# Kernel tuning notes

Measured on AMD Instinct MI355X. Metric: run time of the kernel, lower is better.

The kernel has to match this reference:

```python
import jax, jax.numpy as jnp
import numpy as np

MARGIN = 0.2
PRED_RATE = 1.0
MAX_VIOLATION = True


def t2i_score(images, obj_nums, captions, cap_lens):
    """images: (Bi, O, D); captions: (Bc, W, D).
    For each image, keep only its first obj_nums[i] objects, compute all
    object-word similarities vs every caption, max-pool over objects,
    sum over all W words (incl. padding, as in the torch code), and
    normalize by caption length. Returns (Bi, Bc)."""
    O = images.shape[1]
    # dot[i, c, o, w] = <images[i, o], captions[c, w]>
    dot = jnp.einsum('iod,cwd->icow', images, captions)
    valid = jnp.arange(O)[None, :] < obj_nums[:, None]          # (Bi, O)
    dot = jnp.where(valid[:, None, :, None], dot, -jnp.inf)
    pooled = dot.max(axis=2).sum(axis=2)                        # (Bi, Bc)
    return pooled / cap_lens.astype(pooled.dtype)[None, :]


def setup_inputs() -> dict:
    key = jax.random.key(0)
    ks = jax.random.split(key, 10)
    B, O, W, D = 128, 36, 50, 128
    Op, Wp = 25, 30
    return {
        'im':         jax.random.normal(ks[0], (B, O, D), dtype=jnp.float32),
        'im_l':       jax.random.randint(ks[1], (B,), 1, O + 1, dtype=jnp.int32),
        's':          jax.random.normal(ks[2], (B, W, D), dtype=jnp.float32),
        's_l':        jax.random.randint(ks[3], (B,), 1, W + 1, dtype=jnp.int32),
        'pred':       jax.random.normal(ks[4], (B, Op, D), dtype=jnp.float32),
        'pred_l':     jax.random.randint(ks[5], (B,), 1, Op + 1, dtype=jnp.int32),
        'cap_o_pred': jax.random.normal(ks[6], (B, Op, D), dtype=jnp.float32),
        'cap_o_l':    jax.random.randint(ks[7], (B,), 1, Op + 1, dtype=jnp.int32),
        'c_r_pred':   jax.random.normal(ks[8], (B, Wp, D), dtype=jnp.float32),
        'c_r_l':      jax.random.randint(ks[9], (B,), 1, Wp + 1, dtype=jnp.int32),
    }


def reference(im, im_l, s, s_l, pred, pred_l, cap_o_pred, cap_o_l, c_r_pred, c_r_l):
    scores = (t2i_score(im, im_l, s, s_l)
              + PRED_RATE * t2i_score(pred, pred_l, c_r_pred, c_r_l))  # (B, B)
    B = scores.shape[0]
    diag = jnp.diagonal(scores)
    cost_s = jnp.maximum(MARGIN + scores - diag[:, None], 0.0)
    cost_im = jnp.maximum(MARGIN + scores - diag[None, :], 0.0)
    eye = jnp.eye(B, dtype=bool)
    cost_s = jnp.where(eye, 0.0, cost_s)
    cost_im = jnp.where(eye, 0.0, cost_im)
    if MAX_VIOLATION:
        cost_s = cost_s.max(axis=1)
        cost_im = cost_im.max(axis=0)
    return cost_s.sum() + cost_im.sum()
```

## Files before the change

kernel.cpp:

```cpp
#include <hip/hip_runtime.h>

typedef __bf16 bf16x8 __attribute__((ext_vector_type(8)));
typedef float f32x4 __attribute__((ext_vector_type(4)));
typedef unsigned int u32x4 __attribute__((ext_vector_type(4)));

__device__ __forceinline__ unsigned short f2bf(float f) {
  unsigned int u = __float_as_uint(f);
  u += 0x7FFFu + ((u >> 16) & 1u);
  return (unsigned short)(u >> 16);
}

__device__ __forceinline__ bf16x8 load_frag(const unsigned short* p) {
  u32x4 v = *(const u32x4*)p;
  return __builtin_bit_cast(bf16x8, v);
}

__device__ __forceinline__ void keep(bf16x8& x) {
  asm volatile("" : "+v"(x));
}

__global__ __launch_bounds__(256) void convert_all(
    const float* __restrict__ im, const float* __restrict__ s,
    const float* __restrict__ pred, const float* __restrict__ crp,
    unsigned short* __restrict__ imb, unsigned short* __restrict__ sb,
    unsigned short* __restrict__ pb, unsigned short* __restrict__ cb)
{
  int b = blockIdx.x;
  const float* src; unsigned short* dst; int O, OP, base;
  if (b < 768)       { src = im;   dst = imb; O = 36; OP = 48; base = 0; }
  else if (b < 1568) { src = s;    dst = sb;  O = 50; OP = 50; base = 768; }
  else if (b < 2080) { src = pred; dst = pb;  O = 25; OP = 32; base = 1568; }
  else               { src = crp;  dst = cb;  O = 30; OP = 30; base = 2080; }
  int tid = (b - base) * 256 + (int)threadIdx.x;
  int total = 128 * OP * 32;
  if (tid >= total) return;
  int d4 = tid & 31;
  int o  = (tid >> 5) % OP;
  int bb = tid / (OP * 32);
  unsigned short r0 = 0, r1 = 0, r2 = 0, r3 = 0;
  if (o < O) {
    const float4 v = *(const float4*)(src + ((bb * O + o) << 7) + (d4 << 2));
    r0 = f2bf(v.x); r1 = f2bf(v.y); r2 = f2bf(v.z); r3 = f2bf(v.w);
  }
  ushort4 outv; outv.x = r0; outv.y = r1; outv.z = r2; outv.w = r3;
  *(ushort4*)(dst + (size_t)tid * 4) = outv;
}

template<int MT, int W, int NITER>
__device__ __forceinline__ void t2i_im2(
    const unsigned short* __restrict__ A,
    const unsigned short* __restrict__ Bw,
    const int* __restrict__ obj_l, const int* __restrict__ cap_l,
    float* __restrict__ pooled,
    int vb, float* wmax)
{
  const int i0  = (vb >> 3) * 2;
  const int cg0 = (vb & 7) * 16;
  const int tid = threadIdx.x;
  const int wv = tid >> 6, lane = tid & 63;
  const int quad = lane >> 4, n16 = lane & 15;
  const int ol0 = obj_l[i0], ol1 = obj_l[i0 + 1];

  bf16x8 af[2][MT][4];
#pragma unroll
  for (int im = 0; im < 2; ++im) {
    const unsigned short* Ab =
        A + (((size_t)(i0 + im) * (MT * 16) + n16) << 7) + quad * 8;
#pragma unroll
    for (int t = 0; t < MT; ++t)
#pragma unroll
      for (int sf = 0; sf < 4; ++sf)
        af[im][t][sf] = load_frag(Ab + ((t * 16) << 7) + sf * 32);
  }
#pragma unroll
  for (int im = 0; im < 2; ++im)
#pragma unroll
    for (int t = 0; t < MT; ++t)
#pragma unroll
      for (int sf = 0; sf < 4; ++sf)
        keep(af[im][t][sf]);

  const unsigned short* Bbase = Bw + (((size_t)cg0 * W + n16) << 7) + quad * 8;

  auto ntof = [&](int it) {
    int nt = wv + it * 4;
    return (nt < W) ? nt : nt - W;
  };

  bf16x8 buf[3][4];
  {
    const unsigned short* p0 = Bbase + ((size_t)(ntof(0) * 16) << 7);
#pragma unroll
    for (int sf = 0; sf < 4; ++sf) buf[0][sf] = load_frag(p0 + sf * 32);
  }
  if (NITER > 1) {
    const unsigned short* p1 = Bbase + ((size_t)(ntof(1) * 16) << 7);
#pragma unroll
    for (int sf = 0; sf < 4; ++sf) buf[1][sf] = load_frag(p1 + sf * 32);
  }

#pragma unroll
  for (int it = 0; it < NITER; ++it) {
    if (it + 2 < NITER) {
      const unsigned short* pn = Bbase + ((size_t)(ntof(it + 2) * 16) << 7);
#pragma unroll
      for (int sf = 0; sf < 4; ++sf)
        buf[(it + 2) % 3][sf] = load_frag(pn + sf * 32);
    }
    const int nt = ntof(it);

    f32x4 acc[2][MT];
#pragma unroll
    for (int im = 0; im < 2; ++im)
#pragma unroll
      for (int t = 0; t < MT; ++t) { f32x4 z = {0.f,0.f,0.f,0.f}; acc[im][t] = z; }
#pragma unroll
    for (int sf = 0; sf < 4; ++sf)
#pragma unroll
      for (int im = 0; im < 2; ++im)
#pragma unroll
        for (int t = 0; t < MT; ++t)
          acc[im][t] = __builtin_amdgcn_mfma_f32_16x16x32_bf16(
              af[im][t][sf], buf[it % 3][sf], acc[im][t], 0, 0, 0);

#pragma unroll
    for (int im = 0; im < 2; ++im) {
      const int ol = im ? ol1 : ol0;
      float m = -3.0e38f;
#pragma unroll
      for (int t = 0; t < MT; ++t)
#pragma unroll
        for (int r = 0; r < 4; ++r) {
          int o = t * 16 + quad * 4 + r;
          if (o < ol) m = fmaxf(m, acc[im][t][r]);
        }
      m = fmaxf(m, __shfl_xor(m, 16));
      m = fmaxf(m, __shfl_xor(m, 32));
      if (quad == 0) wmax[im * (16 * W) + nt * 16 + n16] = m;
    }
  }
  __syncthreads();

  if (tid < 32) {
    const int im = tid >> 4, c = tid & 15;
    const float* wp = wmax + im * (16 * W) + c * W;
    float ssum = 0.f;
    for (int w = 0; w < W; ++w) ssum += wp[w];
    const int cc = cg0 + c;
    pooled[((i0 + im) << 7) + cc] = ssum / (float)cap_l[cc];
  }
}

__global__ __launch_bounds__(256, 2) void t2i_both(
    const unsigned short* __restrict__ imb, const unsigned short* __restrict__ sb,
    const unsigned short* __restrict__ pb,  const unsigned short* __restrict__ cb,
    const int* __restrict__ im_l, const int* __restrict__ s_l,
    const int* __restrict__ pred_l, const int* __restrict__ crl,
    float* __restrict__ p1, float* __restrict__ p2)
{
  __shared__ float wmax[2 * 16 * 50];
  if (blockIdx.x < 512)
    t2i_im2<3, 50, 13>(imb, sb, im_l, s_l, p1, (int)blockIdx.x, wmax);
  else
    t2i_im2<2, 30, 8>(pb, cb, pred_l, crl, p2, (int)blockIdx.x - 512, wmax);
}

__global__ __launch_bounds__(256) void loss_kernel(
    const float* __restrict__ p1, const float* __restrict__ p2,
    float* __restrict__ out)
{
  __shared__ float cmax[2][128];
  __shared__ float rmax[2][128];
  __shared__ float wsum[2];
  const int tid = threadIdx.x;
  const int h = tid >> 7, j = tid & 127;

  {
    float cm = -3.0e38f;
    for (int rr = 0; rr < 64; ++rr) {
      const int row = h * 64 + rr;
      const float v = p1[row * 128 + j] + p2[row * 128 + j];
      cm = (row == j) ? cm : fmaxf(cm, v);
    }
    cmax[h][j] = cm;
  }
  {
    float rm = -3.0e38f;
    for (int k = 0; k < 64; ++k) {
      const int c = h * 64 + k;
      const float v = p1[j * 128 + c] + p2[j * 128 + c];
      rm = (c == j) ? rm : fmaxf(rm, v);
    }
    rmax[h][j] = rm;
  }
  __syncthreads();

  float v = 0.f;
  if (tid < 128) {
    const float d  = p1[tid * 129] + p2[tid * 129];
    const float rm = fmaxf(rmax[0][tid], rmax[1][tid]);
    const float cm = fmaxf(cmax[0][tid], cmax[1][tid]);
    v = fmaxf(0.2f + rm - d, 0.f) + fmaxf(0.2f + cm - d, 0.f);
  }
#pragma unroll
  for (int o = 32; o; o >>= 1) v += __shfl_xor(v, o);
  if (tid == 0)  wsum[0] = v;
  if (tid == 64) wsum[1] = v;
  __syncthreads();
  if (tid == 0) out[0] = wsum[0] + wsum[1];
}

extern "C" void kernel_launch(void* const* d_in, const int* in_sizes, int n_in,
                              void* d_out, int out_size, void* d_ws, size_t ws_size,
                              hipStream_t stream)
{
  const float* im     = (const float*)d_in[0];
  const int*   im_l   = (const int*)  d_in[1];
  const float* s      = (const float*)d_in[2];
  const int*   s_l    = (const int*)  d_in[3];
  const float* pred   = (const float*)d_in[4];
  const int*   pred_l = (const int*)  d_in[5];
  const float* crp    = (const float*)d_in[8];
  const int*   crl    = (const int*)  d_in[9];

  char* ws = (char*)d_ws;
  const size_t off_imb = 0;
  const size_t off_sb  = off_imb + (size_t)128 * 48 * 128 * 2;
  const size_t off_pb  = off_sb  + (size_t)128 * 50 * 128 * 2;
  const size_t off_cb  = off_pb  + (size_t)128 * 32 * 128 * 2;
  const size_t off_p1  = off_cb  + (size_t)128 * 30 * 128 * 2;
  const size_t off_p2  = off_p1  + (size_t)128 * 128 * 4;

  unsigned short* imb = (unsigned short*)(ws + off_imb);
  unsigned short* sb  = (unsigned short*)(ws + off_sb);
  unsigned short* pb  = (unsigned short*)(ws + off_pb);
  unsigned short* cb  = (unsigned short*)(ws + off_cb);
  float* p1 = (float*)(ws + off_p1);
  float* p2 = (float*)(ws + off_p2);

  hipLaunchKernelGGL(convert_all, dim3(2560), dim3(256), 0, stream,
                     im, s, pred, crp, imb, sb, pb, cb);
  hipLaunchKernelGGL(t2i_both, dim3(1024), dim3(256), 0, stream,
                     imb, sb, pb, cb, im_l, s_l, pred_l, crl, p1, p2);
  hipLaunchKernelGGL(loss_kernel, dim3(1), dim3(256), 0, stream,
                     p1, p2, (float*)d_out);
}
```

Before: 139.9 us.

## Stage image fragments in LDS instead of registers and raise occupancy

The image-side MFMA operand fragments, previously held in registers for the whole block, are now staged cooperatively into shared memory once and read back from LDS on each MFMA. This frees many VGPRs, so the launch bound moves from 2 to 4 blocks per CU. The caption loop is restructured into a two-buffer ping-pong over fixed strides, replacing the wrapped triple-buffer schedule. In exchange, every MFMA now needs an LDS read, which adds LDS bandwidth pressure and latency, plus an extra barrier after the staging step.

```diff
diff --git a/kernel.cpp b/kernel.cpp
--- a/kernel.cpp
+++ b/kernel.cpp
@@ -15,8 +15,9 @@
   return __builtin_bit_cast(bf16x8, v);
 }
 
-__device__ __forceinline__ void keep(bf16x8& x) {
-  asm volatile("" : "+v"(x));
+__device__ __forceinline__ bf16x8 load_frag_lds(const char* p) {
+  u32x4 v = *(const u32x4*)p;
+  return __builtin_bit_cast(bf16x8, v);
 }
 
 __global__ __launch_bounds__(256) void convert_all(
@@ -46,14 +47,18 @@
   *(ushort4*)(dst + (size_t)tid * 4) = outv;
 }
 
-template<int MT, int W, int NITER>
-__device__ __forceinline__ void t2i_im2(
+template<int MT, int W>
+__device__ __forceinline__ void t2i_lds(
     const unsigned short* __restrict__ A,
     const unsigned short* __restrict__ Bw,
     const int* __restrict__ obj_l, const int* __restrict__ cap_l,
     float* __restrict__ pooled,
-    int vb, float* wmax)
-{
+    int vb, char* lds)
+{
+  constexpr int AFRAGS = 2 * MT * 4;
+  constexpr int ACHUNK = AFRAGS * 64;
+  float* wmax = (float*)(lds + AFRAGS * 1024);
+
   const int i0  = (vb >> 3) * 2;
   const int cg0 = (vb & 7) * 16;
   const int tid = threadIdx.x;
@@ -61,108 +66,135 @@
   const int quad = lane >> 4, n16 = lane & 15;
   const int ol0 = obj_l[i0], ol1 = obj_l[i0 + 1];
 
-  bf16x8 af[2][MT][4];
-#pragma unroll
-  for (int im = 0; im < 2; ++im) {
-    const unsigned short* Ab =
-        A + (((size_t)(i0 + im) * (MT * 16) + n16) << 7) + quad * 8;
-#pragma unroll
-    for (int t = 0; t < MT; ++t)
-#pragma unroll
-      for (int sf = 0; sf < 4; ++sf)
-        af[im][t][sf] = load_frag(Ab + ((t * 16) << 7) + sf * 32);
-  }
-#pragma unroll
-  for (int im = 0; im < 2; ++im)
-#pragma unroll
-    for (int t = 0; t < MT; ++t)
-#pragma unroll
-      for (int sf = 0; sf < 4; ++sf)
-        keep(af[im][t][sf]);
+  for (int c = tid; c < ACHUNK; c += 256) {
+    const int cn = c & 15, cq = (c >> 4) & 3, cs = (c >> 6) & 3;
+    const int rest = c >> 8;
+    const int ct = rest % MT, ci = rest / MT;
+    const unsigned short* g =
+        A + (((size_t)(i0 + ci) * (MT * 16) + ct * 16 + cn) << 7)
+          + cq * 8 + cs * 32;
+    *(u32x4*)(lds + (size_t)c * 16) = *(const u32x4*)g;
+  }
+  __syncthreads();
 
   const unsigned short* Bbase = Bw + (((size_t)cg0 * W + n16) << 7) + quad * 8;
-
-  auto ntof = [&](int it) {
-    int nt = wv + it * 4;
-    return (nt < W) ? nt : nt - W;
-  };
-
-  bf16x8 buf[3][4];
+  const char* abase = lds + lane * 16;
+
+  bf16x8 bA[4], bB[4];
   {
-    const unsigned short* p0 = Bbase + ((size_t)(ntof(0) * 16) << 7);
-#pragma unroll
-    for (int sf = 0; sf < 4; ++sf) buf[0][sf] = load_frag(p0 + sf * 32);
-  }
-  if (NITER > 1) {
-    const unsigned short* p1 = Bbase + ((size_t)(ntof(1) * 16) << 7);
-#pragma unroll
-    for (int sf = 0; sf < 4; ++sf) buf[1][sf] = load_frag(p1 + sf * 32);
-  }
-
-#pragma unroll
-  for (int it = 0; it < NITER; ++it) {
-    if (it + 2 < NITER) {
-      const unsigned short* pn = Bbase + ((size_t)(ntof(it + 2) * 16) << 7);
-#pragma unroll
-      for (int sf = 0; sf < 4; ++sf)
-        buf[(it + 2) % 3][sf] = load_frag(pn + sf * 32);
-    }
-    const int nt = ntof(it);
-
-    f32x4 acc[2][MT];
-#pragma unroll
-    for (int im = 0; im < 2; ++im)
-#pragma unroll
-      for (int t = 0; t < MT; ++t) { f32x4 z = {0.f,0.f,0.f,0.f}; acc[im][t] = z; }
-#pragma unroll
-    for (int sf = 0; sf < 4; ++sf)
-#pragma unroll
-      for (int im = 0; im < 2; ++im)
+    const unsigned short* p = Bbase + ((size_t)(wv * 16) << 7);
+#pragma unroll
+    for (int sf = 0; sf < 4; ++sf) bA[sf] = load_frag(p + sf * 32);
+  }
+
+  for (int nt = wv; nt < W; nt += 8) {
+    const int ntB = nt + 4, ntA2 = nt + 8;
+    if (ntB < W) {
+      const unsigned short* p = Bbase + ((size_t)(ntB * 16) << 7);
+#pragma unroll
+      for (int sf = 0; sf < 4; ++sf) bB[sf] = load_frag(p + sf * 32);
+    }
+
+    {
+      f32x4 acc[2][MT];
+#pragma unroll
+      for (int i2 = 0; i2 < 2; ++i2)
+#pragma unroll
+        for (int t = 0; t < MT; ++t) { f32x4 z = {0.f,0.f,0.f,0.f}; acc[i2][t] = z; }
+#pragma unroll
+      for (int sf = 0; sf < 4; ++sf) {
+#pragma unroll
+        for (int i2 = 0; i2 < 2; ++i2)
+#pragma unroll
+          for (int t = 0; t < MT; ++t) {
+            const bf16x8 af =
+                load_frag_lds(abase + ((i2 * MT + t) * 4 + sf) * 1024);
+            acc[i2][t] = __builtin_amdgcn_mfma_f32_16x16x32_bf16(
+                af, bA[sf], acc[i2][t], 0, 0, 0);
+          }
+      }
+#pragma unroll
+      for (int i2 = 0; i2 < 2; ++i2) {
+        const int ol = i2 ? ol1 : ol0;
+        float m = -3.0e38f;
 #pragma unroll
         for (int t = 0; t < MT; ++t)
-          acc[im][t] = __builtin_amdgcn_mfma_f32_16x16x32_bf16(
-              af[im][t][sf], buf[it % 3][sf], acc[im][t], 0, 0, 0);
-
-#pragma unroll
-    for (int im = 0; im < 2; ++im) {
-      const int ol = im ? ol1 : ol0;
-      float m = -3.0e38f;
-#pragma unroll
-      for (int t = 0; t < MT; ++t)
-#pragma unroll
-        for (int r = 0; r < 4; ++r) {
-          int o = t * 16 + quad * 4 + r;
-          if (o < ol) m = fmaxf(m, acc[im][t][r]);
-        }
-      m = fmaxf(m, __shfl_xor(m, 16));
-      m = fmaxf(m, __shfl_xor(m, 32));
-      if (quad == 0) wmax[im * (16 * W) + nt * 16 + n16] = m;
+#pragma unroll
+          for (int r = 0; r < 4; ++r) {
+            int o = t * 16 + quad * 4 + r;
+            if (o < ol) m = fmaxf(m, acc[i2][t][r]);
+          }
+        m = fmaxf(m, __shfl_xor(m, 16));
+        m = fmaxf(m, __shfl_xor(m, 32));
+        if (quad == 0) wmax[i2 * (16 * W) + nt * 16 + n16] = m;
+      }
+    }
+
+    if (ntA2 < W) {
+      const unsigned short* p = Bbase + ((size_t)(ntA2 * 16) << 7);
+#pragma unroll
+      for (int sf = 0; sf < 4; ++sf) bA[sf] = load_frag(p + sf * 32);
+    }
+
+    if (ntB < W) {
+      f32x4 acc[2][MT];
+#pragma unroll
+      for (int i2 = 0; i2 < 2; ++i2)
+#pragma unroll
+        for (int t = 0; t < MT; ++t) { f32x4 z = {0.f,0.f,0.f,0.f}; acc[i2][t] = z; }
+#pragma unroll
+      for (int sf = 0; sf < 4; ++sf) {
+#pragma unroll
+        for (int i2 = 0; i2 < 2; ++i2)
+#pragma unroll
+          for (int t = 0; t < MT; ++t) {
+            const bf16x8 af =
+                load_frag_lds(abase + ((i2 * MT + t) * 4 + sf) * 1024);
+            acc[i2][t] = __builtin_amdgcn_mfma_f32_16x16x32_bf16(
+                af, bB[sf], acc[i2][t], 0, 0, 0);
+          }
+      }
+#pragma unroll
+      for (int i2 = 0; i2 < 2; ++i2) {
+        const int ol = i2 ? ol1 : ol0;
+        float m = -3.0e38f;
+#pragma unroll
+        for (int t = 0; t < MT; ++t)
+#pragma unroll
+          for (int r = 0; r < 4; ++r) {
+            int o = t * 16 + quad * 4 + r;
+            if (o < ol) m = fmaxf(m, acc[i2][t][r]);
+          }
+        m = fmaxf(m, __shfl_xor(m, 16));
+        m = fmaxf(m, __shfl_xor(m, 32));
+        if (quad == 0) wmax[i2 * (16 * W) + ntB * 16 + n16] = m;
+      }
     }
   }
   __syncthreads();
 
   if (tid < 32) {
-    const int im = tid >> 4, c = tid & 15;
-    const float* wp = wmax + im * (16 * W) + c * W;
+    const int i2 = tid >> 4, c = tid & 15;
+    const float* wp = wmax + i2 * (16 * W) + c * W;
     float ssum = 0.f;
     for (int w = 0; w < W; ++w) ssum += wp[w];
     const int cc = cg0 + c;
-    pooled[((i0 + im) << 7) + cc] = ssum / (float)cap_l[cc];
-  }
-}
-
-__global__ __launch_bounds__(256, 2) void t2i_both(
+    pooled[((i0 + i2) << 7) + cc] = ssum / (float)cap_l[cc];
+  }
+}
+
+__global__ __launch_bounds__(256, 4) void t2i_both(
     const unsigned short* __restrict__ imb, const unsigned short* __restrict__ sb,
     const unsigned short* __restrict__ pb,  const unsigned short* __restrict__ cb,
     const int* __restrict__ im_l, const int* __restrict__ s_l,
     const int* __restrict__ pred_l, const int* __restrict__ crl,
     float* __restrict__ p1, float* __restrict__ p2)
 {
-  __shared__ float wmax[2 * 16 * 50];
+  __shared__ __align__(16) char lds[24 * 1024 + 2 * 16 * 50 * 4];
   if (blockIdx.x < 512)
-    t2i_im2<3, 50, 13>(imb, sb, im_l, s_l, p1, (int)blockIdx.x, wmax);
+    t2i_lds<3, 50>(imb, sb, im_l, s_l, p1, (int)blockIdx.x, lds);
   else
-    t2i_im2<2, 30, 8>(pb, cb, pred_l, crl, p2, (int)blockIdx.x - 512, wmax);
+    t2i_lds<2, 30>(pb, cb, pred_l, crl, p2, (int)blockIdx.x - 512, lds);
 }
 
 __global__ __launch_bounds__(256) void loss_kernel(
```

Result: slower. 155.6 us (+11.2%).
